# Kernel optimization log

Measured on AMD Instinct MI355X. Metric: run time of the kernel, lower is better.

The kernel has to match this reference:

```python
import jax, jax.numpy as jnp
import numpy as np

B = 32
SIZES = [5023, 1256, 314, 79]
NS = [s + 1 for s in SIZES]   # padded vertex counts per level: [5024,1257,315,80]
K = 9
ENC_C = [3, 64, 128, 256]
DEC_C = [256, 128, 64, 3]
LATENT = 256


def _feast(x, nbr, wm, bm, wc, bc, act):
    # x: [B,N,F]; nbr: [N,K] int32 (col 0 = self index)
    xn = jnp.transpose(x[:, nbr, :], (0, 1, 3, 2))          # [B,N,F,K]
    xr = xn - xn[..., :1]                                    # relative to self neighbor
    logits = jnp.einsum('bnfk,of->bnok', xr, wm) + bm[None, None, :, None]  # conv1d(F->K,1)
    perm = jax.nn.softmax(logits, axis=2)                    # softmax over out-channel dim (torch dim=1)
    agg = jnp.einsum('bnfk,bnko->bnfo', xn, perm)            # [B,N,F,K] batched matmul
    Bv, N, F, Kv = agg.shape
    y = act(agg.reshape(Bv, N, F * Kv) @ wc.T + bc)          # linear(F*K -> out)
    mask = jnp.ones((N, 1), y.dtype).at[-1, 0].set(0.0)      # zero out padding vertex
    return y * mask


def _pool(x, L):
    # x: [B,M,F]; L: [Mp,M] -> [B,Mp,F]  (dense form of torch.spmm pooling)
    return jnp.einsum('pm,bmf->bpf', L, x)


def _forward(x, nbrs, Ds, Us, enc_p, dec_p, fce_w, fce_b, fcd_w, fcd_b):
    elu = jax.nn.elu
    ident = lambda v: v
    for i in range(3):
        wm, bm, wc, bc = enc_p[i]
        x = _feast(x, nbrs[i], wm, bm, wc, bc, elu)
        x = _pool(x, Ds[i])
    z = x.reshape(B, -1) @ fce_w.T + fce_b                    # [B, latent]
    x = (z @ fcd_w.T + fcd_b).reshape(B, NS[3], DEC_C[0])
    dec_nbrs = [nbrs[2], nbrs[1], nbrs[0]]
    dec_Us = [Us[2], Us[1], Us[0]]
    acts = [elu, elu, ident]                                  # last dconv uses identity
    for i in range(3):
        x = _pool(x, dec_Us[i])
        wm, bm, wc, bc = dec_p[i]
        x = _feast(x, dec_nbrs[i], wm, bm, wc, bc, acts[i])
    return x


def setup_inputs() -> dict:
    key = jax.random.key(0)
    ks = iter(jax.random.split(key, 64))
    nrm = lambda sh, s=0.05: jax.random.normal(next(ks), sh, dtype=jnp.float32) * s
    inp = {}
    inp['x'] = jax.random.normal(next(ks), (B, NS[0], 3), dtype=jnp.float32)
    for i in range(3):
        n = NS[i]
        nb = jax.random.randint(next(ks), (n, K), 0, n)
        nb = nb.at[:, 0].set(jnp.arange(n))
        inp[f'nbr{i}'] = nb.astype(jnp.int32)
    for i in range(3):
        cols = jax.random.randint(next(ks), (NS[i + 1],), 0, NS[i])
        inp[f'D{i}'] = jax.nn.one_hot(cols, NS[i], dtype=jnp.float32)   # sparse-like pooling
        cols_u = jax.random.randint(next(ks), (NS[i],), 0, NS[i + 1])
        inp[f'U{i}'] = jax.nn.one_hot(cols_u, NS[i + 1], dtype=jnp.float32)
    for i in range(3):
        fi, fo = ENC_C[i], ENC_C[i + 1]
        inp[f'e{i}_wm'] = nrm((K, fi)); inp[f'e{i}_bm'] = jnp.zeros((K,), jnp.float32)
        inp[f'e{i}_wc'] = nrm((fo, fi * K)); inp[f'e{i}_bc'] = jnp.zeros((fo,), jnp.float32)
    inp['fce_w'] = nrm((LATENT, NS[3] * ENC_C[3])); inp['fce_b'] = jnp.zeros((LATENT,), jnp.float32)
    inp['fcd_w'] = nrm((NS[3] * DEC_C[0], LATENT)); inp['fcd_b'] = jnp.zeros((NS[3] * DEC_C[0],), jnp.float32)
    for i in range(3):
        fi, fo = DEC_C[i], DEC_C[i + 1]
        inp[f'd{i}_wm'] = nrm((K, fi)); inp[f'd{i}_bm'] = jnp.zeros((K,), jnp.float32)
        inp[f'd{i}_wc'] = nrm((fo, fi * K)); inp[f'd{i}_bc'] = jnp.zeros((fo,), jnp.float32)
    return inp


def reference(x, nbr0, nbr1, nbr2, D0, D1, D2, U0, U1, U2,
              e0_wm, e0_bm, e0_wc, e0_bc, e1_wm, e1_bm, e1_wc, e1_bc,
              e2_wm, e2_bm, e2_wc, e2_bc, fce_w, fce_b, fcd_w, fcd_b,
              d0_wm, d0_bm, d0_wc, d0_bc, d1_wm, d1_bm, d1_wc, d1_bc,
              d2_wm, d2_bm, d2_wc, d2_bc):
    nbrs = [nbr0, nbr1, nbr2]
    Ds = [D0, D1, D2]
    Us = [U0, U1, U2]
    enc_p = [(e0_wm, e0_bm, e0_wc, e0_bc), (e1_wm, e1_bm, e1_wc, e1_bc), (e2_wm, e2_bm, e2_wc, e2_bc)]
    dec_p = [(d0_wm, d0_bm, d0_wc, d0_bc), (d1_wm, d1_bm, d1_wc, d1_bc), (d2_wm, d2_bm, d2_wc, d2_bc)]
    return _forward(x, nbrs, Ds, Us, enc_p, dec_p, fce_w, fce_b, fcd_w, fcd_b)
```

## Files before the change

kernel.cpp:

```cpp
#include <hip/hip_runtime.h>
#include <cstddef>

#define KN 9
typedef unsigned short u16;
typedef unsigned int u32;
typedef __attribute__((ext_vector_type(8))) short short8;
typedef __attribute__((ext_vector_type(4))) float f32x4;

__device__ inline u16 f2b(float f) {
    union { float f; u32 u; } v; v.f = f;
    u32 r = v.u + 0x7FFFu + ((v.u >> 16) & 1u);
    return (u16)(r >> 16);
}
__device__ inline float b2f(u16 h) {
    union { u32 u; float f; } v; v.u = ((u32)h) << 16; return v.f;
}

__device__ inline int xcd_swz(int bid, int n) {
    int q = n >> 3, r = n & 7;
    int x = bid & 7, pos = bid >> 3;
    return (x < r ? x * (q + 1) : r * (q + 1) + (x - r) * q) + pos;
}

__global__ void extract_idx_all(
    const float* __restrict__ D0, const float* __restrict__ D1, const float* __restrict__ D2,
    const float* __restrict__ U0, const float* __restrict__ U1, const float* __restrict__ U2,
    int* __restrict__ iD0, int* __restrict__ iD1, int* __restrict__ iD2,
    int* __restrict__ iU0, int* __restrict__ iU1, int* __restrict__ iU2)
{
    int blk = blockIdx.x;
    const float* L; int M; int* out; int p;
    if      (blk < 1257) { L = D0; M = 5024; out = iD0; p = blk; }
    else if (blk < 1572) { L = D1; M = 1257; out = iD1; p = blk - 1257; }
    else if (blk < 1652) { L = D2; M = 315;  out = iD2; p = blk - 1572; }
    else if (blk < 6676) { L = U0; M = 1257; out = iU0; p = blk - 1652; }
    else if (blk < 7933) { L = U1; M = 315;  out = iU1; p = blk - 6676; }
    else                 { L = U2; M = 80;   out = iU2; p = blk - 7933; }
    const float* row = L + (size_t)p * M;
    for (int m = threadIdx.x; m < M; m += 256)
        if (row[m] > 0.5f) out[p] = m;
}

__device__ inline void wcr_one(const float* __restrict__ wc, u16* __restrict__ out, int t, int F) {
    int FK = F * KN;
    int c = t / FK, rem = t - c * FK, j = rem / F, f = rem - j * F;
    out[t] = f2b(wc[(size_t)c * FK + f * KN + j]);
}
__device__ inline void wg_one(const float* __restrict__ wc, u16* __restrict__ out, int t, int F, int C) {
    int n = t / F, f = t - n * F;
    int j = n / C, c = n - j * C;
    out[t] = f2b(wc[(size_t)c * (F * KN) + f * KN + j]);
}
__device__ inline void ccw_one(const float* __restrict__ wm, u16* __restrict__ out, int t, int F) {
    int n = t / F, f = t - n * F;
    out[t] = (n < KN) ? f2b(wm[n * F + f]) : (u16)0;
}
__global__ void cvt_weights(
    const float* __restrict__ e1_wc, const float* __restrict__ e2_wc,
    const float* __restrict__ d0_wc, const float* __restrict__ d1_wc,
    const float* __restrict__ e1_wm, const float* __restrict__ e2_wm,
    const float* __restrict__ d0_wm, const float* __restrict__ d1_wm,
    const float* __restrict__ d2_wm, const float* __restrict__ d2_wc,
    u16* __restrict__ wcrE1, u16* __restrict__ wcrE2,
    u16* __restrict__ wg0, u16* __restrict__ wg1,
    u16* __restrict__ ccwE1, u16* __restrict__ ccwE2,
    u16* __restrict__ ccwD0, u16* __restrict__ ccwD1,
    u16* __restrict__ w3, float* __restrict__ zbuf)
{
    int t = blockIdx.x * 256 + threadIdx.x;
    if (t < 73728)  { wcr_one(e1_wc, wcrE1, t, 64);       return; } t -= 73728;
    if (t < 294912) { wcr_one(e2_wc, wcrE2, t, 128);      return; } t -= 294912;
    if (t < 294912) { wg_one(d0_wc, wg0, t, 256, 128);    return; } t -= 294912;
    if (t < 73728)  { wg_one(d1_wc, wg1, t, 128, 64);     return; } t -= 73728;
    if (t < 4096)   { ccw_one(e1_wm, ccwE1, t, 64);       return; } t -= 4096;
    if (t < 8192)   { ccw_one(e2_wm, ccwE2, t, 128);      return; } t -= 8192;
    if (t < 16384)  { ccw_one(d0_wm, ccwD0, t, 256);      return; } t -= 16384;
    if (t < 8192)   { ccw_one(d1_wm, ccwD1, t, 128);      return; } t -= 8192;
    if (t < 4096) {
        int n = t >> 6, k = t & 63;
        float v = 0.f;
        if (n < KN) v = d2_wm[n * 64 + k];
        else if (n >= 9 && n < 36) {
            int cj = n - 9, j = cj / 3, c = cj - j * 3;
            v = d2_wc[(size_t)c * 576 + k * KN + j];
        }
        w3[t] = f2b(v);
        return;
    } t -= 4096;
    if (t < 8192) zbuf[t] = 0.f;
}

__global__ void compose_tables(
    const int* __restrict__ nbr0, const int* __restrict__ nbr1, const int* __restrict__ nbr2,
    const int* __restrict__ idxD1, const int* __restrict__ idxD2,
    const int* __restrict__ idxU0, const int* __restrict__ idxU1, const int* __restrict__ idxU2,
    int* __restrict__ nbrD1, int* __restrict__ nbrD2,
    int* __restrict__ nbrU2, int* __restrict__ nbrU1, int* __restrict__ nbrU0,
    int* __restrict__ maskE1, int* __restrict__ maskE2)
{
    int t = blockIdx.x * 256 + threadIdx.x;
    if (t < 2835)  { int p = t / 9, j = t - p * 9; nbrD1[p * 12 + j] = nbr1[idxD1[p] * 9 + j]; return; } t -= 2835;
    if (t < 720)   { int p = t / 9, j = t - p * 9; nbrD2[p * 12 + j] = nbr2[idxD2[p] * 9 + j]; return; } t -= 720;
    if (t < 2835)  { int p = t / 9, j = t - p * 9; nbrU2[p * 12 + j] = idxU2[nbr2[p * 9 + j]]; return; } t -= 2835;
    if (t < 11313) { int p = t / 9, j = t - p * 9; nbrU1[p * 12 + j] = idxU1[nbr1[p * 9 + j]]; return; } t -= 11313;
    if (t < 45216) { int p = t / 9, j = t - p * 9; nbrU0[p * 12 + j] = idxU0[nbr0[p * 9 + j]]; return; } t -= 45216;
    if (t < 315)   { maskE1[t] = (idxD1[t] == 1256) ? 1 : 0; return; } t -= 315;
    if (t < 80)    { maskE2[t] = (idxD2[t] == 314) ? 1 : 0; }
}

template<int NW, int OS>
__global__ __launch_bounds__(256) void cc_gemm(
    const u16* __restrict__ A, const u16* __restrict__ W,
    float* __restrict__ out, int M, int F)
{
    __shared__ u16 As[64 * 72];
    __shared__ u16 Ws[64 * 72];
    int tid = threadIdx.x;
    int mT = blockIdx.x * 64;
    int wid = tid >> 6, lane = tid & 63;
    int wr = wid >> 1, wcq = wid & 1;
    int r = lane & 15, g = lane >> 4;
    f32x4 acc[2][2];
    #pragma unroll
    for (int i = 0; i < 2; ++i)
        #pragma unroll
        for (int j = 0; j < 2; ++j)
            acc[i][j] = (f32x4){0.f, 0.f, 0.f, 0.f};

    for (int k0 = 0; k0 < F; k0 += 64) {
        #pragma unroll
        for (int h = 0; h < 2; ++h) {
            int gi = tid + h * 256;
            int m = gi >> 3, kg = gi & 7;
            uint4 va = {0u, 0u, 0u, 0u};
            int row = mT + m;
            if (row < M) va = *(const uint4*)(A + (size_t)row * F + k0 + kg * 8);
            *(uint4*)&As[m * 72 + kg * 8] = va;
            *(uint4*)&Ws[m * 72 + kg * 8] = *(const uint4*)(W + (size_t)m * F + k0 + kg * 8);
        }
        __syncthreads();
        #pragma unroll
        for (int S = 0; S < 2; ++S) {
            short8 af[2], bf[2];
            #pragma unroll
            for (int R = 0; R < 2; ++R)
                af[R] = *(const short8*)&As[(wr * 32 + R * 16 + r) * 72 + S * 32 + g * 8];
            #pragma unroll
            for (int C2 = 0; C2 < 2; ++C2)
                bf[C2] = *(const short8*)&Ws[(wcq * 32 + C2 * 16 + r) * 72 + S * 32 + g * 8];
            #pragma unroll
            for (int R = 0; R < 2; ++R)
                #pragma unroll
                for (int C2 = 0; C2 < 2; ++C2)
                    acc[R][C2] = __builtin_amdgcn_mfma_f32_16x16x32_bf16(af[R], bf[C2], acc[R][C2], 0, 0, 0);
        }
        __syncthreads();
    }
    #pragma unroll
    for (int R = 0; R < 2; ++R)
        #pragma unroll
        for (int C2 = 0; C2 < 2; ++C2)
            #pragma unroll
            for (int q = 0; q < 4; ++q) {
                int mm = mT + wr * 32 + R * 16 + g * 4 + q;
                int nn = wcq * 32 + C2 * 16 + r;
                if (mm < M && nn < NW)
                    out[(size_t)mm * OS + nn] = acc[R][C2][q];
            }
}

__global__ __launch_bounds__(256) void cc_gemmT(
    const u16* __restrict__ A, const u16* __restrict__ W,
    float* __restrict__ CCT, float* __restrict__ GWT, int M)
{
    __shared__ u16 As[64 * 72];
    __shared__ u16 Ws[64 * 72];
    int tid = threadIdx.x;
    int mT = blockIdx.x * 64;
    int wid = tid >> 6, lane = tid & 63;
    int wr = wid >> 1, wcq = wid & 1;
    int r = lane & 15, g = lane >> 4;
    f32x4 acc[2][2];
    #pragma unroll
    for (int i = 0; i < 2; ++i)
        #pragma unroll
        for (int j = 0; j < 2; ++j)
            acc[i][j] = (f32x4){0.f, 0.f, 0.f, 0.f};

    {
        #pragma unroll
        for (int h = 0; h < 2; ++h) {
            int gi = tid + h * 256;
            int m = gi >> 3, kg = gi & 7;
            uint4 va = {0u, 0u, 0u, 0u};
            int row = mT + m;
            if (row < M) va = *(const uint4*)(A + (size_t)row * 64 + kg * 8);
            *(uint4*)&As[m * 72 + kg * 8] = va;
            *(uint4*)&Ws[m * 72 + kg * 8] = *(const uint4*)(W + (size_t)m * 64 + kg * 8);
        }
        __syncthreads();
        #pragma unroll
        for (int S = 0; S < 2; ++S) {
            short8 af[2], bf[2];
            #pragma unroll
            for (int R = 0; R < 2; ++R)
                af[R] = *(const short8*)&As[(wr * 32 + R * 16 + r) * 72 + S * 32 + g * 8];
            #pragma unroll
            for (int C2 = 0; C2 < 2; ++C2)
                bf[C2] = *(const short8*)&Ws[(wcq * 32 + C2 * 16 + r) * 72 + S * 32 + g * 8];
            #pragma unroll
            for (int R = 0; R < 2; ++R)
                #pragma unroll
                for (int C2 = 0; C2 < 2; ++C2)
                    acc[R][C2] = __builtin_amdgcn_mfma_f32_16x16x32_bf16(af[R], bf[C2], acc[R][C2], 0, 0, 0);
        }
    }
    #pragma unroll
    for (int R = 0; R < 2; ++R)
        #pragma unroll
        for (int C2 = 0; C2 < 2; ++C2)
            #pragma unroll
            for (int q = 0; q < 4; ++q) {
                int mm = mT + wr * 32 + R * 16 + g * 4 + q;
                if (mm >= M) continue;
                int nn = wcq * 32 + C2 * 16 + r;
                if (nn >= 36) continue;
                int b = mm / 1257, p = mm - b * 1257;
                float val = acc[R][C2][q];
                if (nn < 9) {
                    CCT[((size_t)p * 9 + nn) * 32 + b] = val;
                } else {
                    int cj = nn - 9, j = cj / 3, c = cj - j * 3;
                    GWT[(size_t)p * 864 + j * 96 + b * 3 + c] = val;
                }
            }
}

template<int ACT, int MASK>
__global__ __launch_bounds__(256) void lin_gemm(
    const u16* __restrict__ A, const u16* __restrict__ W,
    const float* __restrict__ bias, u16* __restrict__ Y,
    const int* __restrict__ maskT,
    int M, int K, int N, int P)
{
    __shared__ u16 As[2][64 * 72];
    __shared__ u16 Ws[2][64 * 72];
    int tid = threadIdx.x;
    int mT = blockIdx.x * 64, nT = blockIdx.y * 64;
    int wid = tid >> 6, lane = tid & 63;
    int wr = wid >> 1, wcq = wid & 1;
    int r = lane & 15, g = lane >> 4;
    int lm = tid >> 3, lkg = tid & 7;
    f32x4 acc[2][2];
    #pragma unroll
    for (int i = 0; i < 2; ++i)
        #pragma unroll
        for (int j = 0; j < 2; ++j)
            acc[i][j] = (f32x4){0.f, 0.f, 0.f, 0.f};

    uint4 ra[2], rw[2];
    #pragma unroll
    for (int h = 0; h < 2; ++h) {
        int m = lm + h * 32;
        int row = mT + m;
        uint4 z; z.x = z.y = z.z = z.w = 0u;
        ra[h] = (row < M) ? *(const uint4*)(A + (size_t)row * K + lkg * 8) : z;
        rw[h] = *(const uint4*)(W + (size_t)(nT + m) * K + lkg * 8);
    }
    #pragma unroll
    for (int h = 0; h < 2; ++h) {
        int m = lm + h * 32;
        *(uint4*)&As[0][m * 72 + lkg * 8] = ra[h];
        *(uint4*)&Ws[0][m * 72 + lkg * 8] = rw[h];
    }

    int cur = 0;
    for (int k0 = 0; k0 < K; k0 += 64) {
        __syncthreads();
        bool more = (k0 + 64 < K);
        if (more) {
            int kn = k0 + 64;
            #pragma unroll
            for (int h = 0; h < 2; ++h) {
                int m = lm + h * 32;
                int row = mT + m;
                uint4 z; z.x = z.y = z.z = z.w = 0u;
                ra[h] = (row < M) ? *(const uint4*)(A + (size_t)row * K + kn + lkg * 8) : z;
                rw[h] = *(const uint4*)(W + (size_t)(nT + m) * K + kn + lkg * 8);
            }
        }
        #pragma unroll
        for (int S = 0; S < 2; ++S) {
            short8 af[2], bf[2];
            #pragma unroll
            for (int R = 0; R < 2; ++R)
                af[R] = *(const short8*)&As[cur][(wr * 32 + R * 16 + r) * 72 + S * 32 + g * 8];
            #pragma unroll
            for (int C2 = 0; C2 < 2; ++C2)
                bf[C2] = *(const short8*)&Ws[cur][(wcq * 32 + C2 * 16 + r) * 72 + S * 32 + g * 8];
            #pragma unroll
            for (int R = 0; R < 2; ++R)
                #pragma unroll
                for (int C2 = 0; C2 < 2; ++C2)
                    acc[R][C2] = __builtin_amdgcn_mfma_f32_16x16x32_bf16(af[R], bf[C2], acc[R][C2], 0, 0, 0);
        }
        if (more) {
            #pragma unroll
            for (int h = 0; h < 2; ++h) {
                int m = lm + h * 32;
                *(uint4*)&As[cur ^ 1][m * 72 + lkg * 8] = ra[h];
                *(uint4*)&Ws[cur ^ 1][m * 72 + lkg * 8] = rw[h];
            }
        }
        cur ^= 1;
    }

    #pragma unroll
    for (int R = 0; R < 2; ++R)
        #pragma unroll
        for (int C2 = 0; C2 < 2; ++C2)
            #pragma unroll
            for (int q = 0; q < 4; ++q) {
                int mm = mT + wr * 32 + R * 16 + g * 4 + q;
                if (mm >= M) continue;
                int nn = nT + wcq * 32 + C2 * 16 + r;
                float v = acc[R][C2][q];
                if (bias) v += bias[nn];
                if (ACT == 1) v = v > 0.f ? v : expm1f(v);
                if (MASK) { if (maskT[mm % P] != 0) v = 0.f; }
                Y[(size_t)mm * N + nn] = f2b(v);
            }
}

__global__ __launch_bounds__(256) void fce_mfma(
    const u16* __restrict__ A, const float* __restrict__ Wf,
    const float* __restrict__ bias, float* __restrict__ z)
{
    __shared__ u16 As[32 * 72];
    __shared__ u16 Ws[64 * 72];
    int tid = threadIdx.x;
    int nT = blockIdx.x * 64;
    int kbase = blockIdx.y * 256;
    int wv = tid >> 6, lane = tid & 63;
    int r = lane & 15, g = lane >> 4;
    int m = tid >> 3, kg = tid & 7;
    f32x4 acc[2];
    acc[0] = (f32x4){0.f, 0.f, 0.f, 0.f};
    acc[1] = (f32x4){0.f, 0.f, 0.f, 0.f};

    for (int ks = 0; ks < 4; ++ks) {
        int k0 = kbase + ks * 64;
        *(uint4*)&As[m * 72 + kg * 8] = *(const uint4*)(A + (size_t)m * 20480 + k0 + kg * 8);
        #pragma unroll
        for (int h = 0; h < 2; ++h) {
            int row = m + h * 32;
            const float* wr2 = Wf + (size_t)(nT + row) * 20480 + k0 + kg * 8;
            float4 w0 = *(const float4*)(wr2);
            float4 w1 = *(const float4*)(wr2 + 4);
            u16 o[8] = { f2b(w0.x), f2b(w0.y), f2b(w0.z), f2b(w0.w),
                         f2b(w1.x), f2b(w1.y), f2b(w1.z), f2b(w1.w) };
            *(uint4*)&Ws[row * 72 + kg * 8] = *(const uint4*)o;
        }
        __syncthreads();
        #pragma unroll
        for (int S = 0; S < 2; ++S) {
            short8 bfr = *(const short8*)&Ws[(wv * 16 + r) * 72 + S * 32 + g * 8];
            #pragma unroll
            for (int R = 0; R < 2; ++R) {
                short8 af = *(const short8*)&As[(R * 16 + r) * 72 + S * 32 + g * 8];
                acc[R] = __builtin_amdgcn_mfma_f32_16x16x32_bf16(af, bfr, acc[R], 0, 0, 0);
            }
        }
        __syncthreads();
    }
    #pragma unroll
    for (int R = 0; R < 2; ++R)
        #pragma unroll
        for (int q = 0; q < 4; ++q) {
            int mm = R * 16 + g * 4 + q;
            int nn = nT + wv * 16 + r;
            float v = acc[R][q];
            if (blockIdx.y == 0) v += bias[nn];
            atomicAdd(&z[mm * 256 + nn], v);
        }
}

__global__ __launch_bounds__(256) void fcd_mfma(
    const float* __restrict__ Af, const float* __restrict__ Wf,
    const float* __restrict__ bias, u16* __restrict__ Y)
{
    __shared__ u16 As[64 * 72];
    __shared__ u16 Ws[64 * 72];
    int tid = threadIdx.x;
    int nT = blockIdx.x * 64;
    int wid = tid >> 6, lane = tid & 63;
    int wr = wid >> 1, wcq = wid & 1;
    int r = lane & 15, g = lane >> 4;
    int m = tid >> 3, kg = tid & 7;
    f32x4 acc[2][2];
    #pragma unroll
    for (int i = 0; i < 2; ++i)
        #pragma unroll
        for (int j = 0; j < 2; ++j)
            acc[i][j] = (f32x4){0.f, 0.f, 0.f, 0.f};

    for (int k0 = 0; k0 < 256; k0 += 64) {
        {
            const float* ar = Af + (size_t)m * 256 + k0 + kg * 8;
            float4 a0 = *(const float4*)(ar);
            float4 a1 = *(const float4*)(ar + 4);
            u16 o[8] = { f2b(a0.x), f2b(a0.y), f2b(a0.z), f2b(a0.w),
                         f2b(a1.x), f2b(a1.y), f2b(a1.z), f2b(a1.w) };
            *(uint4*)&As[m * 72 + kg * 8] = *(const uint4*)o;
            uint4 z4; z4.x = z4.y = z4.z = z4.w = 0u;
            *(uint4*)&As[(m + 32) * 72 + kg * 8] = z4;
        }
        #pragma unroll
        for (int h = 0; h < 2; ++h) {
            int row = m + h * 32;
            const float* wr2 = Wf + (size_t)(nT + row) * 256 + k0 + kg * 8;
            float4 w0 = *(const float4*)(wr2);
            float4 w1 = *(const float4*)(wr2 + 4);
            u16 o[8] = { f2b(w0.x), f2b(w0.y), f2b(w0.z), f2b(w0.w),
                         f2b(w1.x), f2b(w1.y), f2b(w1.z), f2b(w1.w) };
            *(uint4*)&Ws[row * 72 + kg * 8] = *(const uint4*)o;
        }
        __syncthreads();
        #pragma unroll
        for (int S = 0; S < 2; ++S) {
            short8 af[2], bf[2];
            #pragma unroll
            for (int R = 0; R < 2; ++R)
                af[R] = *(const short8*)&As[(wr * 32 + R * 16 + r) * 72 + S * 32 + g * 8];
            #pragma unroll
            for (int C2 = 0; C2 < 2; ++C2)
                bf[C2] = *(const short8*)&Ws[(wcq * 32 + C2 * 16 + r) * 72 + S * 32 + g * 8];
            #pragma unroll
            for (int R = 0; R < 2; ++R)
                #pragma unroll
                for (int C2 = 0; C2 < 2; ++C2)
                    acc[R][C2] = __builtin_amdgcn_mfma_f32_16x16x32_bf16(af[R], bf[C2], acc[R][C2], 0, 0, 0);
        }
        __syncthreads();
    }
    #pragma unroll
    for (int R = 0; R < 2; ++R)
        #pragma unroll
        for (int C2 = 0; C2 < 2; ++C2)
            #pragma unroll
            for (int q = 0; q < 4; ++q) {
                int mm = wr * 32 + R * 16 + g * 4 + q;
                if (mm >= 32) continue;
                int nn = nT + wcq * 32 + C2 * 16 + r;
                float v = acc[R][C2][q] + bias[nn];
                Y[(size_t)mm * 20480 + nn] = f2b(v);
            }
}

template<int F>
__global__ __launch_bounds__(256) void feast_agg(
    const u16* __restrict__ x, const float* __restrict__ cc,
    const int* __restrict__ nbrT, const float* __restrict__ bm,
    u16* __restrict__ agg, int Pin, int P, int Mtot)
{
    constexpr int FC = F / 64;
    __shared__ float s_p[4][81];
    __shared__ int s_nb[4][KN];
    int tid = threadIdx.x, wid = tid >> 6, lane = tid & 63;
    int row = xcd_swz(blockIdx.x, gridDim.x) * 4 + wid;
    bool aw = row < Mtot;
    int b = 0, p = 0;
    if (aw) { b = row / P; p = row - b * P; }
    if (aw && lane < KN) s_nb[wid][lane] = b * Pin + nbrT[p * 12 + lane];
    __syncthreads();

    if (aw && lane < KN) {
        int j = lane;
        const float* c0 = cc + (size_t)s_nb[wid][0] * 16;
        const float* cj = cc + (size_t)s_nb[wid][j] * 16;
        float L[KN];
        #pragma unroll
        for (int i = 0; i < KN; ++i) L[i] = bm[i] + cj[i] - c0[i];
        float mx = L[0];
        #pragma unroll
        for (int i = 1; i < KN; ++i) mx = fmaxf(mx, L[i]);
        float s = 0.f;
        #pragma unroll
        for (int i = 0; i < KN; ++i) { L[i] = __expf(L[i] - mx); s += L[i]; }
        float inv = 1.f / s;
        #pragma unroll
        for (int i = 0; i < KN; ++i) s_p[wid][i * KN + j] = L[i] * inv;
    }
    __syncthreads();

    if (aw) {
        float xn[KN][FC];
        #pragma unroll
        for (int i = 0; i < KN; ++i) {
            const u16* xr = x + (size_t)s_nb[wid][i] * F;
            #pragma unroll
            for (int c = 0; c < FC; ++c) xn[i][c] = b2f(xr[lane + c * 64]);
        }
        #pragma unroll
        for (int j = 0; j < KN; ++j) {
            float a[FC];
            #pragma unroll
            for (int c = 0; c < FC; ++c) a[c] = 0.f;
            #pragma unroll
            for (int i = 0; i < KN; ++i) {
                float pv = s_p[wid][i * KN + j];
                #pragma unroll
                for (int c = 0; c < FC; ++c) a[c] += xn[i][c] * pv;
            }
            u16* orow = agg + (size_t)row * (KN * F) + j * F;
            #pragma unroll
            for (int c = 0; c < FC; ++c) orow[lane + c * 64] = f2b(a[c]);
        }
    }
}

template<int C>
__global__ __launch_bounds__(256) void mix_feast(
    const u16* __restrict__ G, const float* __restrict__ cc,
    const int* __restrict__ nbrT, const float* __restrict__ bm,
    const float* __restrict__ bc, u16* __restrict__ y,
    int Pin, int P, int Mtot)
{
    constexpr int GS = KN * C;
    constexpr int CC_ = C / 64;
    __shared__ float s_p[4][81];
    __shared__ int s_nb[4][KN];
    int tid = threadIdx.x, wid = tid >> 6, lane = tid & 63;
    int row = xcd_swz(blockIdx.x, gridDim.x) * 4 + wid;
    bool aw = row < Mtot;
    int b = 0, p = 0;
    if (aw) { b = row / P; p = row - b * P; }
    if (aw && lane < KN) s_nb[wid][lane] = b * Pin + nbrT[p * 12 + lane];
    __syncthreads();

    if (aw && lane < KN) {
        int j = lane;
        const float* c0 = cc + (size_t)s_nb[wid][0] * 16;
        const float* cj = cc + (size_t)s_nb[wid][j] * 16;
        float L[KN];
        #pragma unroll
        for (int i = 0; i < KN; ++i) L[i] = bm[i] + cj[i] - c0[i];
        float mx = L[0];
        #pragma unroll
        for (int i = 1; i < KN; ++i) mx = fmaxf(mx, L[i]);
        float s = 0.f;
        #pragma unroll
        for (int i = 0; i < KN; ++i) { L[i] = __expf(L[i] - mx); s += L[i]; }
        float inv = 1.f / s;
        #pragma unroll
        for (int i = 0; i < KN; ++i) s_p[wid][i * KN + j] = L[i] * inv;
    }
    __syncthreads();

    if (aw) {
        float acc[CC_];
        #pragma unroll
        for (int c = 0; c < CC_; ++c) acc[c] = bc[lane + c * 64];
        #pragma unroll
        for (int i = 0; i < KN; ++i) {
            const u16* gr = G + (size_t)s_nb[wid][i] * GS;
            float pv[KN];
            #pragma unroll
            for (int j = 0; j < KN; ++j) pv[j] = s_p[wid][i * KN + j];
            #pragma unroll
            for (int j = 0; j < KN; ++j)
                #pragma unroll
                for (int c = 0; c < CC_; ++c)
                    acc[c] += pv[j] * b2f(gr[j * C + lane + c * 64]);
        }
        #pragma unroll
        for (int c = 0; c < CC_; ++c) {
            float v = acc[c];
            v = v > 0.f ? v : expm1f(v);
            if (p == P - 1) v = 0.f;
            y[(size_t)row * C + lane + c * 64] = f2b(v);
        }
    }
}

__global__ __launch_bounds__(256) void feast_e0(
    const float* __restrict__ x, const int* __restrict__ nbr,
    const int* __restrict__ sel,
    const float* __restrict__ wm, const float* __restrict__ bm,
    const float* __restrict__ wcw, const float* __restrict__ bc,
    u16* __restrict__ y,
    int Nin, int P, int Nlevel, int Mtot)
{
    constexpr int F = 3, C = 64, FS = 4, Q = 27;
    __shared__ float s_wm[KN * FS];
    __shared__ float s_wc[C * Q];
    __shared__ float s_bm[KN];
    __shared__ float s_xn[4][KN * FS];
    __shared__ float s_lg[4][81];
    __shared__ float s_pm[4][81];
    __shared__ float s_ag[4][Q];
    __shared__ int   s_idx[4][KN];

    int tid = threadIdx.x, wid = tid >> 6, lane = tid & 63;
    for (int t = tid; t < KN * F; t += 256) { int i = t / F, f = t - i * F; s_wm[i * FS + f] = wm[t]; }
    for (int t = tid; t < C * Q; t += 256) s_wc[t] = wcw[t];
    if (tid < KN) s_bm[tid] = bm[tid];

    int wg = xcd_swz(blockIdx.x, gridDim.x) * 4 + wid;
    bool aw = wg < Mtot;
    int b = 0, p = 0, n = 0;
    if (aw) {
        b = wg / P; p = wg - b * P;
        n = sel[p];
    }
    if (aw && lane < KN) s_idx[wid][lane] = nbr[n * KN + lane];
    __syncthreads();

    if (aw) {
        const float* xb = x + (size_t)b * Nin * F;
        for (int t = lane; t < KN * F; t += 64) {
            int i = t / F, f = t - i * F;
            s_xn[wid][i * FS + f] = xb[(size_t)s_idx[wid][i] * F + f];
        }
    }
    __syncthreads();

    if (aw) {
        for (int pr = lane; pr < 81; pr += 64) {
            int i = pr / KN, j = pr - i * KN;
            float acc = s_bm[i];
            for (int f = 0; f < F; ++f)
                acc += (s_xn[wid][j * FS + f] - s_xn[wid][f]) * s_wm[i * FS + f];
            s_lg[wid][pr] = acc;
        }
    }
    __syncthreads();

    if (aw && lane < KN) {
        int j = lane;
        float mx = -1e30f;
        #pragma unroll
        for (int i = 0; i < KN; ++i) mx = fmaxf(mx, s_lg[wid][i * KN + j]);
        float sm = 0.f, ev[KN];
        #pragma unroll
        for (int i = 0; i < KN; ++i) { ev[i] = __expf(s_lg[wid][i * KN + j] - mx); sm += ev[i]; }
        float inv = 1.f / sm;
        #pragma unroll
        for (int i = 0; i < KN; ++i) s_pm[wid][i * KN + j] = ev[i] * inv;
    }
    __syncthreads();

    if (aw) {
        for (int t = lane; t < Q; t += 64) {
            int f = t / KN, j = t - f * KN;
            float acc = 0.f;
            #pragma unroll
            for (int i = 0; i < KN; ++i) acc += s_xn[wid][i * FS + f] * s_pm[wid][i * KN + j];
            s_ag[wid][t] = acc;
        }
    }
    __syncthreads();

    if (aw) {
        int c = lane;
        float acc = 0.f;
        #pragma unroll
        for (int q = 0; q < Q; ++q)
            acc += s_wc[c * Q + q] * s_ag[wid][q];
        float val = acc + bc[c];
        val = val > 0.f ? val : expm1f(val);
        if (n == Nlevel - 1) val = 0.f;
        y[(size_t)wg * C + c] = f2b(val);
    }
}

__global__ __launch_bounds__(256) void mix_d2t(
    const float* __restrict__ CCT, const float* __restrict__ GWT,
    const int* __restrict__ nbrT,
    const float* __restrict__ bm9, const float* __restrict__ bc3,
    float* __restrict__ out)
{
    __shared__ float s_out[8][32][3];
    int tid = threadIdx.x, wid = tid >> 6, lane = tid & 63;
    int sub = lane >> 5, b = lane & 31;
    int vbase = xcd_swz(blockIdx.x, gridDim.x) * 8;
    int v = vbase + wid * 2 + sub;

    int nbi[KN];
    #pragma unroll
    for (int i = 0; i < KN; ++i) nbi[i] = nbrT[v * 12 + i];
    float bmr[KN];
    #pragma unroll
    for (int i = 0; i < KN; ++i) bmr[i] = bm9[i];

    float cc0[KN];
    {
        const float* c0 = CCT + (size_t)nbi[0] * 9 * 32 + b;
        #pragma unroll
        for (int f = 0; f < KN; ++f) cc0[f] = c0[f * 32];
    }
    float a0 = bc3[0], a1 = bc3[1], a2 = bc3[2];
    #pragma unroll
    for (int j = 0; j < KN; ++j) {
        const float* cj = CCT + (size_t)nbi[j] * 9 * 32 + b;
        float L[KN];
        #pragma unroll
        for (int i = 0; i < KN; ++i) L[i] = bmr[i] + cj[i * 32] - cc0[i];
        float mx = L[0];
        #pragma unroll
        for (int i = 1; i < KN; ++i) mx = fmaxf(mx, L[i]);
        float sm = 0.f;
        #pragma unroll
        for (int i = 0; i < KN; ++i) { L[i] = __expf(L[i] - mx); sm += L[i]; }
        float inv = 1.f / sm;
        #pragma unroll
        for (int i = 0; i < KN; ++i) {
            float pv = L[i] * inv;
            const float* g = GWT + (size_t)nbi[i] * 864 + j * 96 + b * 3;
            a0 += pv * g[0];
            a1 += pv * g[1];
            a2 += pv * g[2];
        }
    }
    if (v == 5023) { a0 = 0.f; a1 = 0.f; a2 = 0.f; }
    s_out[wid * 2 + sub][b][0] = a0;
    s_out[wid * 2 + sub][b][1] = a1;
    s_out[wid * 2 + sub][b][2] = a2;
    __syncthreads();
    {
        int bb = tid >> 3, vi = tid & 7;
        float* dst = out + ((size_t)bb * 5024 + vbase + vi) * 3;
        dst[0] = s_out[vi][bb][0];
        dst[1] = s_out[vi][bb][1];
        dst[2] = s_out[vi][bb][2];
    }
}

extern "C" void kernel_launch(void* const* d_in, const int* in_sizes, int n_in,
                              void* d_out, int out_size, void* d_ws, size_t ws_size,
                              hipStream_t stream)
{
    const float* x     = (const float*)d_in[0];
    const int*   nbr0  = (const int*)d_in[1];
    const int*   nbr1  = (const int*)d_in[2];
    const int*   nbr2  = (const int*)d_in[3];
    const float* D0    = (const float*)d_in[4];
    const float* U0    = (const float*)d_in[5];
    const float* D1    = (const float*)d_in[6];
    const float* U1    = (const float*)d_in[7];
    const float* D2    = (const float*)d_in[8];
    const float* U2    = (const float*)d_in[9];
    const float* e0_wm = (const float*)d_in[10]; const float* e0_bm = (const float*)d_in[11];
    const float* e0_wc = (const float*)d_in[12]; const float* e0_bc = (const float*)d_in[13];
    const float* e1_wm = (const float*)d_in[14]; const float* e1_bm = (const float*)d_in[15];
    const float* e1_wc = (const float*)d_in[16]; const float* e1_bc = (const float*)d_in[17];
    const float* e2_wm = (const float*)d_in[18]; const float* e2_bm = (const float*)d_in[19];
    const float* e2_wc = (const float*)d_in[20]; const float* e2_bc = (const float*)d_in[21];
    const float* fce_w = (const float*)d_in[22]; const float* fce_b = (const float*)d_in[23];
    const float* fcd_w = (const float*)d_in[24]; const float* fcd_b = (const float*)d_in[25];
    const float* d0_wm = (const float*)d_in[26]; const float* d0_bm = (const float*)d_in[27];
    const float* d0_wc = (const float*)d_in[28]; const float* d0_bc = (const float*)d_in[29];
    const float* d1_wm = (const float*)d_in[30]; const float* d1_bm = (const float*)d_in[31];
    const float* d1_wc = (const float*)d_in[32]; const float* d1_bc = (const float*)d_in[33];
    const float* d2_wm = (const float*)d_in[34]; const float* d2_bm = (const float*)d_in[35];
    const float* d2_wc = (const float*)d_in[36]; const float* d2_bc = (const float*)d_in[37];

    char* w = (char*)d_ws;
    int* idxD0 = (int*)(w);
    int* idxD1 = idxD0 + 1257;
    int* idxD2 = idxD1 + 315;
    int* idxU0 = idxD2 + 80;
    int* idxU1 = idxU0 + 5024;
    int* idxU2 = idxU1 + 1257;
    int* nbrD1  = (int*)(w + 33024);
    int* nbrD2  = (int*)(w + 48144);
    int* nbrU2  = (int*)(w + 51984);
    int* nbrU1  = (int*)(w + 67104);
    int* nbrU0  = (int*)(w + 127440);
    int* maskE1 = (int*)(w + 368640);
    int* maskE2 = (int*)(w + 369920);
    u16* wcrE1 = (u16*)(w + 370432);
    u16* wcrE2 = (u16*)(w + 517888);
    u16* wg0   = (u16*)(w + 1107712);
    u16* wg1   = (u16*)(w + 1697536);
    u16* ccwE1 = (u16*)(w + 1844992);
    u16* ccwE2 = (u16*)(w + 1853184);
    u16* ccwD0 = (u16*)(w + 1869568);
    u16* ccwD1 = (u16*)(w + 1902336);
    u16* w3    = (u16*)(w + 1918720);
    float* zbuf = (float*)(w + 1926912);

    u16*   X1   = (u16*)  (w + 2097152);
    float* CC1  = (float*)(w + 7245824);
    u16*   AGG1 = (u16*)  (w + 9820160);
    u16*   X2   = (u16*)  (w + 21432320);
    float* CC2  = (float*)(w + 24012800);
    u16*   AGG2 = (u16*)  (w + 24657920);
    u16*   X3   = (u16*)  (w + 2097152);
    u16*   X3P  = (u16*)  (w + 3407872);
    float* CCD0 = (float*)(w + 4718592);
    u16*   G0   = (u16*)  (w + 4882432);
    u16*   XD1P = (u16*)  (w + 10780672);
    float* CCD1 = (float*)(w + 13361152);
    u16*   G1   = (u16*)  (w + 14006272);
    u16*   XD2P = (u16*)  (w + 25618432);
    float* CCT  = (float*)(w + 30767104);
    float* GWT  = (float*)(w + 32215168);

    extract_idx_all<<<8248, 256, 0, stream>>>(D0, D1, D2, U0, U1, U2,
                                              idxD0, idxD1, idxD2, idxU0, idxU1, idxU2);
    cvt_weights<<<3072, 256, 0, stream>>>(e1_wc, e2_wc, d0_wc, d1_wc,
                                          e1_wm, e2_wm, d0_wm, d1_wm, d2_wm, d2_wc,
                                          wcrE1, wcrE2, wg0, wg1,
                                          ccwE1, ccwE2, ccwD0, ccwD1, w3, zbuf);
    compose_tables<<<248, 256, 0, stream>>>(nbr0, nbr1, nbr2,
                                            idxD1, idxD2, idxU0, idxU1, idxU2,
                                            nbrD1, nbrD2, nbrU2, nbrU1, nbrU0,
                                            maskE1, maskE2);

    feast_e0<<<10056, 256, 0, stream>>>(x, nbr0, idxD0, e0_wm, e0_bm, e0_wc, e0_bc,
                                        X1, 5024, 1257, 5024, 40224);
    cc_gemm<16, 16><<<629, 256, 0, stream>>>(X1, ccwE1, CC1, 40224, 64);
    feast_agg<64><<<2520, 256, 0, stream>>>(X1, CC1, nbrD1, e1_bm, AGG1, 1257, 315, 10080);
    lin_gemm<1, 1><<<dim3(158, 2), 256, 0, stream>>>(AGG1, wcrE1, e1_bc, X2, maskE1,
                                                     10080, 576, 128, 315);
    cc_gemm<16, 16><<<158, 256, 0, stream>>>(X2, ccwE2, CC2, 10080, 128);
    feast_agg<128><<<640, 256, 0, stream>>>(X2, CC2, nbrD2, e2_bm, AGG2, 315, 80, 2560);
    lin_gemm<1, 1><<<dim3(40, 4), 256, 0, stream>>>(AGG2, wcrE2, e2_bc, X3, maskE2,
                                                    2560, 1152, 256, 80);

    fce_mfma<<<dim3(4, 80), 256, 0, stream>>>(X3, fce_w, fce_b, zbuf);
    fcd_mfma<<<320, 256, 0, stream>>>(zbuf, fcd_w, fcd_b, X3P);

    cc_gemm<16, 16><<<40, 256, 0, stream>>>(X3P, ccwD0, CCD0, 2560, 256);
    lin_gemm<0, 0><<<dim3(40, 18), 256, 0, stream>>>(X3P, wg0, nullptr, G0, nullptr,
                                                     2560, 256, 1152, 1);
    mix_feast<128><<<2520, 256, 0, stream>>>(G0, CCD0, nbrU2, d0_bm, d0_bc, XD1P,
                                             80, 315, 10080);
    cc_gemm<16, 16><<<158, 256, 0, stream>>>(XD1P, ccwD1, CCD1, 10080, 128);
    lin_gemm<0, 0><<<dim3(158, 9), 256, 0, stream>>>(XD1P, wg1, nullptr, G1, nullptr,
                                                     10080, 128, 576, 1);
    mix_feast<64><<<10056, 256, 0, stream>>>(G1, CCD1, nbrU1, d1_bm, d1_bc, XD2P,
                                             315, 1257, 40224);
    cc_gemmT<<<629, 256, 0, stream>>>(XD2P, w3, CCT, GWT, 40224);
    mix_d2t<<<628, 256, 0, stream>>>(CCT, GWT, nbrU0, d2_bm, d2_bc, (float*)d_out);
}
```

Measured before the change: 285.7 us.

## Split-K the encoder linear GEMMs with atomic accumulation and separate epilogue

Replaces the two encoder lin_gemm launches, whose grids are small (316 and 160 blocks), with a split-K MFMA GEMM that spreads the K dimension over a third grid axis and accumulates into fp32 buffers with atomicAdd. A new elementwise kernel then applies bias, ELU, padding mask and the bf16 conversion. A zeroing kernel clears both fp32 buffers up front. The aim is more blocks to fill the GPU on these GEMMs, paid for with atomic traffic, two extra launches and extra fp32 memory round trips.

```diff
diff --git a/kernel.cpp b/kernel.cpp
--- a/kernel.cpp
+++ b/kernel.cpp
@@ -39,6 +39,12 @@
     const float* row = L + (size_t)p * M;
     for (int m = threadIdx.x; m < M; m += 256)
         if (row[m] > 0.5f) out[p] = m;
+}
+
+__global__ void zero_f32(float4* __restrict__ p, int n4)
+{
+    int t = blockIdx.x * 256 + threadIdx.x;
+    if (t < n4) p[t] = (float4){0.f, 0.f, 0.f, 0.f};
 }
 
 __device__ inline void wcr_one(const float* __restrict__ wc, u16* __restrict__ out, int t, int F) {
@@ -330,6 +336,94 @@
                 if (MASK) { if (maskT[mm % P] != 0) v = 0.f; }
                 Y[(size_t)mm * N + nn] = f2b(v);
             }
+}
+
+__global__ __launch_bounds__(256) void lin_gemm_sk(
+    const u16* __restrict__ A, const u16* __restrict__ W,
+    float* __restrict__ Yf, int M, int K, int N, int KSTEPS)
+{
+    __shared__ u16 As[64 * 72];
+    __shared__ u16 Ws[64 * 72];
+    int tid = threadIdx.x;
+    int mT = blockIdx.x * 64, nT = blockIdx.y * 64;
+    int kbase = blockIdx.z * KSTEPS * 64;
+    int wid = tid >> 6, lane = tid & 63;
+    int wr = wid >> 1, wcq = wid & 1;
+    int r = lane & 15, g = lane >> 4;
+    f32x4 acc[2][2];
+    #pragma unroll
+    for (int i = 0; i < 2; ++i)
+        #pragma unroll
+        for (int j = 0; j < 2; ++j)
+            acc[i][j] = (f32x4){0.f, 0.f, 0.f, 0.f};
+
+    for (int s = 0; s < KSTEPS; ++s) {
+        int k0 = kbase + s * 64;
+        #pragma unroll
+        for (int h = 0; h < 2; ++h) {
+            int gi = tid + h * 256;
+            int m = gi >> 3, kg = gi & 7;
+            uint4 va = {0u, 0u, 0u, 0u};
+            int row = mT + m;
+            if (row < M) va = *(const uint4*)(A + (size_t)row * K + k0 + kg * 8);
+            *(uint4*)&As[m * 72 + kg * 8] = va;
+            *(uint4*)&Ws[m * 72 + kg * 8] = *(const uint4*)(W + (size_t)(nT + m) * K + k0 + kg * 8);
+        }
+        __syncthreads();
+        #pragma unroll
+        for (int S = 0; S < 2; ++S) {
+            short8 af[2], bf[2];
+            #pragma unroll
+            for (int R = 0; R < 2; ++R)
+                af[R] = *(const short8*)&As[(wr * 32 + R * 16 + r) * 72 + S * 32 + g * 8];
+            #pragma unroll
+            for (int C2 = 0; C2 < 2; ++C2)
+                bf[C2] = *(const short8*)&Ws[(wcq * 32 + C2 * 16 + r) * 72 + S * 32 + g * 8];
+            #pragma unroll
+            for (int R = 0; R < 2; ++R)
+                #pragma unroll
+                for (int C2 = 0; C2 < 2; ++C2)
+                    acc[R][C2] = __builtin_amdgcn_mfma_f32_16x16x32_bf16(af[R], bf[C2], acc[R][C2], 0, 0, 0);
+        }
+        __syncthreads();
+    }
+    #pragma unroll
+    for (int R = 0; R < 2; ++R)
+        #pragma unroll
+        for (int C2 = 0; C2 < 2; ++C2)
+            #pragma unroll
+            for (int q = 0; q < 4; ++q) {
+                int mm = mT + wr * 32 + R * 16 + g * 4 + q;
+                if (mm >= M) continue;
+                int nn = nT + wcq * 32 + C2 * 16 + r;
+                atomicAdd(&Yf[(size_t)mm * N + nn], acc[R][C2][q]);
+            }
+}
+
+__global__ __launch_bounds__(256) void elu_mask_cvt(
+    const float* __restrict__ Yf, const float* __restrict__ bias,
+    const int* __restrict__ maskT, u16* __restrict__ Y,
+    int M, int N, int P)
+{
+    int t = blockIdx.x * 256 + threadIdx.x;
+    int tot = (M * N) >> 2;
+    if (t >= tot) return;
+    int e0 = t * 4;
+    int m = e0 / N, n0 = e0 - m * N;
+    float4 v = ((const float4*)Yf)[t];
+    float o0 = v.x + bias[n0];
+    float o1 = v.y + bias[n0 + 1];
+    float o2 = v.z + bias[n0 + 2];
+    float o3 = v.w + bias[n0 + 3];
+    o0 = o0 > 0.f ? o0 : expm1f(o0);
+    o1 = o1 > 0.f ? o1 : expm1f(o1);
+    o2 = o2 > 0.f ? o2 : expm1f(o2);
+    o3 = o3 > 0.f ? o3 : expm1f(o3);
+    if (maskT[m % P] != 0) { o0 = 0.f; o1 = 0.f; o2 = 0.f; o3 = 0.f; }
+    uint2 o;
+    o.x = (u32)f2b(o0) | ((u32)f2b(o1) << 16);
+    o.y = (u32)f2b(o2) | ((u32)f2b(o3) << 16);
+    ((uint2*)Y)[t] = o;
 }
 
 __global__ __launch_bounds__(256) void fce_mfma(
@@ -806,6 +900,8 @@
     u16*   XD2P = (u16*)  (w + 25618432);
     float* CCT  = (float*)(w + 30767104);
     float* GWT  = (float*)(w + 32215168);
+    float* X2F  = (float*)(w + 36559360);
+    float* X3F  = (float*)(w + 41720320);
 
     extract_idx_all<<<8248, 256, 0, stream>>>(D0, D1, D2, U0, U1, U2,
                                               idxD0, idxD1, idxD2, idxU0, idxU1, idxU2);
@@ -817,17 +913,18 @@
                                             idxD1, idxD2, idxU0, idxU1, idxU2,
                                             nbrD1, nbrD2, nbrU2, nbrU1, nbrU0,
                                             maskE1, maskE2);
+    zero_f32<<<1900, 256, 0, stream>>>((float4*)X2F, 486400);
 
     feast_e0<<<10056, 256, 0, stream>>>(x, nbr0, idxD0, e0_wm, e0_bm, e0_wc, e0_bc,
                                         X1, 5024, 1257, 5024, 40224);
     cc_gemm<16, 16><<<629, 256, 0, stream>>>(X1, ccwE1, CC1, 40224, 64);
     feast_agg<64><<<2520, 256, 0, stream>>>(X1, CC1, nbrD1, e1_bm, AGG1, 1257, 315, 10080);
-    lin_gemm<1, 1><<<dim3(158, 2), 256, 0, stream>>>(AGG1, wcrE1, e1_bc, X2, maskE1,
-                                                     10080, 576, 128, 315);
+    lin_gemm_sk<<<dim3(158, 2, 3), 256, 0, stream>>>(AGG1, wcrE1, X2F, 10080, 576, 128, 3);
+    elu_mask_cvt<<<1260, 256, 0, stream>>>(X2F, e1_bc, maskE1, X2, 10080, 128, 315);
     cc_gemm<16, 16><<<158, 256, 0, stream>>>(X2, ccwE2, CC2, 10080, 128);
     feast_agg<128><<<640, 256, 0, stream>>>(X2, CC2, nbrD2, e2_bm, AGG2, 315, 80, 2560);
-    lin_gemm<1, 1><<<dim3(40, 4), 256, 0, stream>>>(AGG2, wcrE2, e2_bc, X3, maskE2,
-                                                    2560, 1152, 256, 80);
+    lin_gemm_sk<<<dim3(40, 4, 6), 256, 0, stream>>>(AGG2, wcrE2, X3F, 2560, 1152, 256, 3);
+    elu_mask_cvt<<<640, 256, 0, stream>>>(X3F, e2_bc, maskE2, X3, 2560, 256, 80);
 
     fce_mfma<<<dim3(4, 80), 256, 0, stream>>>(X3, fce_w, fce_b, zbuf);
     fcd_mfma<<<320, 256, 0, stream>>>(zbuf, fcd_w, fcd_b, X3P);
```

New measurement: 256.1 us. 1.12x faster.
